# Kernel optimization log

Hardware: AMD Instinct MI355X
Metric: run time of the kernel (lower is better)

Reference implementation:

```python
import jax, jax.numpy as jnp
import numpy as np
import math

D = 256      # d_model
HEADS = 8
PTS = 4      # num_points
L = 6        # num_layers
FF = 1024    # dim_feedforward
B = 8
HS, WS = 100, 100  # feature map -> N = 10000
HD = D // HEADS


def setup_inputs() -> dict:
    key = jax.random.key(0)
    ks = jax.random.split(key, 8)
    w = lambda k, shape, s: jax.random.normal(k, shape, jnp.float32) * s
    z = lambda *shape: jnp.zeros(shape, jnp.float32)
    return {
        "src": jax.random.normal(ks[0], (B, HS * WS, D), jnp.float32),
        "Wv": w(ks[1], (L, D, D), 0.02), "bv": z(L, D),
        "Woff": w(ks[2], (L, D, HEADS * PTS * 2), 0.01), "boff": z(L, HEADS * PTS * 2),
        "Wa": w(ks[3], (L, D, HEADS * PTS), 0.02), "ba": z(L, HEADS * PTS),
        "Wo": w(ks[4], (L, D, D), 0.02), "bo": z(L, D),
        "W1": w(ks[5], (L, D, FF), 0.02), "b1": z(L, FF),
        "W2": w(ks[6], (L, FF, D), 0.02), "b2": z(L, D),
        "g1": jnp.ones((L, D)), "be1": z(L, D),
        "g2": jnp.ones((L, D)), "be2": z(L, D),
        "H": HS, "W": WS,
    }


def pos_encoding_2d(d_model, H, W):
    # standard 2D sine encoding: first half of channels encode y, second half x
    half = d_model // 2
    freqs = jnp.exp(-math.log(10000.0) * jnp.arange(0, half, 2, dtype=jnp.float32) / half)
    ya = jnp.arange(H, dtype=jnp.float32)[:, None] * freqs[None, :]
    xa = jnp.arange(W, dtype=jnp.float32)[:, None] * freqs[None, :]
    pe_y = jnp.stack([jnp.sin(ya), jnp.cos(ya)], -1).reshape(H, half)
    pe_x = jnp.stack([jnp.sin(xa), jnp.cos(xa)], -1).reshape(W, half)
    pe = jnp.concatenate([
        jnp.broadcast_to(pe_y[:, None, :], (H, W, half)),
        jnp.broadcast_to(pe_x[None, :, :], (H, W, half))], -1)
    return pe.reshape(H * W, d_model)


def layer_norm(x, g, b, eps=1e-5):
    m = x.mean(-1, keepdims=True)
    v = ((x - m) ** 2).mean(-1, keepdims=True)
    return (x - m) * jax.lax.rsqrt(v + eps) * g + b


def deform_attn(q, Wv, bv, Woff, boff, Wa, ba, Wo, bo, H, W):
    # single-scale Deformable-DETR attention; q: [B, N, D], N = H*W
    Bq, N, _ = q.shape
    v = (q @ Wv + bv).reshape(Bq, N, HEADS, HD)
    off = (q @ Woff + boff).reshape(Bq, N, HEADS, PTS, 2)          # (dx, dy) in pixels
    attn = jax.nn.softmax((q @ Wa + ba).reshape(Bq, N, HEADS, PTS), axis=-1)
    # reference points: normalized grid cell centers
    ys, xs = jnp.meshgrid(jnp.arange(H, dtype=jnp.float32),
                          jnp.arange(W, dtype=jnp.float32), indexing='ij')
    ref = jnp.stack([(xs.reshape(-1) + 0.5) / W, (ys.reshape(-1) + 0.5) / H], -1)  # [N,2]
    loc = ref[None, :, None, None, :] + off / jnp.array([W, H], jnp.float32)       # [B,N,h,P,2]
    # pixel coords, align_corners=False; border padding via clamping
    px = loc[..., 0] * W - 0.5
    py = loc[..., 1] * H - 0.5
    x0 = jnp.floor(px); y0 = jnp.floor(py)
    wx = px - x0; wy = py - y0
    x0i = jnp.clip(x0.astype(jnp.int32), 0, W - 1); x1i = jnp.clip(x0i + 1, 0, W - 1)
    y0i = jnp.clip(y0.astype(jnp.int32), 0, H - 1); y1i = jnp.clip(y0i + 1, 0, H - 1)
    vbh = v.transpose(0, 2, 1, 3).reshape(Bq * HEADS, N, HD)       # [B*h, N, hd]
    flat = lambda yi, xi: (yi * W + xi).transpose(0, 2, 1, 3).reshape(Bq * HEADS, N * PTS)
    gather = jax.vmap(lambda val, idx: val[idx])                   # [B*h, N*P, hd]
    wxr = wx.transpose(0, 2, 1, 3).reshape(Bq * HEADS, N * PTS, 1)
    wyr = wy.transpose(0, 2, 1, 3).reshape(Bq * HEADS, N * PTS, 1)
    s = (gather(vbh, flat(y0i, x0i)) * (1 - wxr) * (1 - wyr)
         + gather(vbh, flat(y0i, x1i)) * wxr * (1 - wyr)
         + gather(vbh, flat(y1i, x0i)) * (1 - wxr) * wyr
         + gather(vbh, flat(y1i, x1i)) * wxr * wyr)
    s = s.reshape(Bq, HEADS, N, PTS, HD)
    out = jnp.einsum('bhnp,bhnpd->bhnd', attn.transpose(0, 2, 1, 3), s)
    out = out.transpose(0, 2, 1, 3).reshape(Bq, N, D)
    return out @ Wo + bo


def reference(src, Wv, bv, Woff, boff, Wa, ba, Wo, bo, W1, b1, W2, b2,
              g1, be1, g2, be2, H, W):
    x = src + pos_encoding_2d(D, H, W)[None]
    for i in range(L):
        a = deform_attn(x, Wv[i], bv[i], Woff[i], boff[i], Wa[i], ba[i], Wo[i], bo[i], H, W)
        x = layer_norm(x + a, g1[i], be1[i])
        h = jax.nn.gelu(x @ W1[i] + b1[i], approximate=False)
        x = layer_norm(x + (h @ W2[i] + b2[i]), g2[i], be2[i])
    return x
```

## Files before the change

### kernel.cpp

```cpp
#include <hip/hip_runtime.h>
#include <hip/hip_bf16.h>
#include <math.h>

#define Bq   8
#define NPix 10000
#define HH   100
#define WW   100
#define Dm   256
#define NH   8
#define HD   32
#define PTS  4
#define FFd  1024
#define Lnum 6
#define Mrows (Bq * NPix)

typedef short bf16x8 __attribute__((ext_vector_type(8)));
typedef float f32x4 __attribute__((ext_vector_type(4)));
typedef unsigned int uint2v __attribute__((ext_vector_type(2)));

__device__ __forceinline__ float bf2f(unsigned short u) {
    return __uint_as_float(((unsigned)u) << 16);
}
__device__ __forceinline__ unsigned short f2bf(float f) {
    unsigned x = __float_as_uint(f);
    return (unsigned short)((x + 0x7fffu + ((x >> 16) & 1u)) >> 16);
}
__device__ __forceinline__ float gelu_t(float v) {
    float z = 1.5957691216f * (v + 0.044715f * v * v * v);
    float e = __expf(z);
    float th = 1.0f - 2.0f / (e + 1.0f);
    return 0.5f * v * (1.0f + th);
}

__global__ __launch_bounds__(256) void pos_add_kernel(
    const float* __restrict__ src, float* __restrict__ x, short* __restrict__ xb)
{
    int idx = blockIdx.x * 256 + threadIdx.x;
    int c = idx & (Dm - 1);
    int n = (idx >> 8) % NPix;
    int cc = c;
    float coord;
    if (c < 128) { coord = (float)(n / WW); }
    else         { coord = (float)(n % WW); cc = c - 128; }
    int j = cc >> 1;
    float f = __expf(-logf(10000.0f) * (2.0f * (float)j) / 128.0f);
    float arg = coord * f;
    float pe = (cc & 1) ? cosf(arg) : sinf(arg);
    float val = src[idx] + pe;
    x[idx] = val;
    xb[idx] = (short)f2bf(val);
}

__global__ __launch_bounds__(256) void repack_kernel(
    const float* __restrict__ W, short* __restrict__ Wt,
    int K, int N, int outLstride, int nOff)
{
    __shared__ float t[64][65];
    int l  = blockIdx.z;
    int k0 = blockIdx.y * 64, n0 = blockIdx.x * 64;
    const float* Wl = W + (size_t)l * K * N;
    for (int i = threadIdx.x; i < 64 * 64; i += 256) {
        int kk = i >> 6, nn = i & 63;
        float val = 0.0f;
        if (k0 + kk < K && n0 + nn < N) val = Wl[(size_t)(k0 + kk) * N + (n0 + nn)];
        t[kk][nn] = val;
    }
    __syncthreads();
    for (int i = threadIdx.x; i < 64 * 64; i += 256) {
        int nn = i >> 6, kk = i & 63;
        if (n0 + nn < N && k0 + kk < K)
            Wt[(size_t)l * outLstride + (size_t)(nOff + n0 + nn) * K + (k0 + kk)]
                = (short)f2bf(t[kk][nn]);
    }
}

__global__ void bcat_kernel(const float* __restrict__ bv,
                            const float* __restrict__ boff,
                            const float* __restrict__ ba,
                            float* __restrict__ bcat)
{
    int l = blockIdx.x, c = threadIdx.x;
    float v;
    if (c < 256)      v = bv[l * 256 + c];
    else if (c < 320) v = boff[l * 64 + (c - 256)];
    else              v = ba[l * 32 + (c - 320)];
    bcat[l * 352 + c] = v;
}

template<int KI, int MODE>
__global__ __launch_bounds__(256) void gemm_mfma_kernel(
    const short* __restrict__ A, const short* __restrict__ Bt,
    const float* __restrict__ bias, short* __restrict__ Cv,
    float* __restrict__ C2,
    int M, int Nc, int ldc)
{
    constexpr int K = KI * 64;
    __shared__ short As[128 * 64];
    __shared__ short Bs[128 * 64];
    const int tid = threadIdx.x;

    int nwg  = gridDim.x * gridDim.y;
    int orig = blockIdx.y * gridDim.x + blockIdx.x;
    int xcd  = orig & 7, pos = orig >> 3;
    int q = nwg >> 3, r = nwg & 7;
    int flat = (xcd < r ? xcd * (q + 1) : r * (q + 1) + (xcd - r) * q) + pos;
    const int bm = (flat / gridDim.x) * 128;
    const int bn = (flat % gridDim.x) * 128;

    const int w = tid >> 6, l = tid & 63;
    const int wr = (w >> 1) * 64, wc = (w & 1) * 64;
    const int rl = tid >> 3;
    const int cl = tid & 7;
    const int lr = l & 15, lq = l >> 4;

    const short* pA[4]; const short* pB[4];
    #pragma unroll
    for (int p = 0; p < 4; ++p) {
        int row = p * 32 + rl;
        int sc  = cl ^ (row & 7);
        int ga  = bm + row; if (ga > M - 1) ga = M - 1;
        pA[p] = A + (size_t)ga * K + sc * 8;
        int gb  = bn + row; if (gb > Nc - 1) gb = Nc - 1;
        pB[p] = Bt + (size_t)gb * K + sc * 8;
    }

    int xoff[2][4], woff[2][4];
    #pragma unroll
    for (int ks = 0; ks < 2; ++ks)
        #pragma unroll
        for (int m = 0; m < 4; ++m) {
            int ra = wr + m * 16 + lr;
            xoff[ks][m] = ra * 64 + (((ks * 4 + lq) ^ (ra & 7))) * 8;
            int rb = wc + m * 16 + lr;
            woff[ks][m] = rb * 64 + (((ks * 4 + lq) ^ (rb & 7))) * 8;
        }

    f32x4 acc[4][4];
    #pragma unroll
    for (int m = 0; m < 4; ++m)
        #pragma unroll
        for (int n = 0; n < 4; ++n)
            #pragma unroll
            for (int j = 0; j < 4; ++j) acc[m][n][j] = 0.0f;

    #pragma unroll
    for (int kc = 0; kc < KI; ++kc) {
        #pragma unroll
        for (int p = 0; p < 4; ++p) {
            __builtin_amdgcn_global_load_lds((const void*)pA[p],
                (void*)&As[(p * 32 + w * 8) * 64], 16, 0, 0);
            pA[p] += 64;
            __builtin_amdgcn_global_load_lds((const void*)pB[p],
                (void*)&Bs[(p * 32 + w * 8) * 64], 16, 0, 0);
            pB[p] += 64;
        }
        __syncthreads();

        #pragma unroll
        for (int ks = 0; ks < 2; ++ks) {
            bf16x8 wf[4], xf[4];
            #pragma unroll
            for (int m = 0; m < 4; ++m) wf[m] = *(const bf16x8*)&Bs[woff[ks][m]];
            #pragma unroll
            for (int n = 0; n < 4; ++n) xf[n] = *(const bf16x8*)&As[xoff[ks][n]];
            #pragma unroll
            for (int m = 0; m < 4; ++m)
                #pragma unroll
                for (int n = 0; n < 4; ++n)
                    acc[m][n] = __builtin_amdgcn_mfma_f32_16x16x32_bf16(
                        wf[m], xf[n], acc[m][n], 0, 0, 0);
        }
        __syncthreads();
    }

    float4 bi[4];
    #pragma unroll
    for (int m = 0; m < 4; ++m) {
        int colBase = bn + wc + m * 16 + lq * 4;
        bi[m] = (MODE == 2 && colBase >= Nc) ? float4{0,0,0,0}
                                             : *(const float4*)&bias[colBase];
    }

    #pragma unroll
    for (int n = 0; n < 4; ++n) {
        int rr = bm + wr + n * 16 + lr;
        if (rr >= M) continue;
        #pragma unroll
        for (int m = 0; m < 4; ++m) {
            int colBase = bn + wc + m * 16 + lq * 4;
            if (MODE == 2 && colBase >= Nc) continue;
            float o0 = acc[m][n][0] + bi[m].x;
            float o1 = acc[m][n][1] + bi[m].y;
            float o2 = acc[m][n][2] + bi[m].z;
            float o3 = acc[m][n][3] + bi[m].w;
            if (MODE == 0) {
                o0 = gelu_t(o0); o1 = gelu_t(o1); o2 = gelu_t(o2); o3 = gelu_t(o3);
                uint2v pk;
                pk.x = (unsigned)f2bf(o0) | ((unsigned)f2bf(o1) << 16);
                pk.y = (unsigned)f2bf(o2) | ((unsigned)f2bf(o3) << 16);
                *(uint2v*)&Cv[(size_t)rr * ldc + colBase] = pk;
            } else {
                if (colBase < 256) {
                    uint2v pk;
                    pk.x = (unsigned)f2bf(o0) | ((unsigned)f2bf(o1) << 16);
                    pk.y = (unsigned)f2bf(o2) | ((unsigned)f2bf(o3) << 16);
                    *(uint2v*)&Cv[(size_t)rr * 256 + colBase] = pk;
                } else {
                    float4 pk; pk.x = o0; pk.y = o1; pk.z = o2; pk.w = o3;
                    *(float4*)&C2[(size_t)rr * 96 + (colBase - 256)] = pk;
                }
            }
        }
    }
}

template<int KI>
__global__ __launch_bounds__(512) void gemm_ln_kernel(
    const short* __restrict__ A, const short* __restrict__ Bt,
    const float* __restrict__ bias,
    const float* __restrict__ gw, const float* __restrict__ bw,
    float* __restrict__ x, short* __restrict__ xb,
    int M)
{
    constexpr int K = KI * 64;
    __shared__ short As[128 * 64];
    __shared__ short Bs[256 * 64];
    const int tid = threadIdx.x;
    const int bm = blockIdx.x * 128;
    const int w = tid >> 6, l = tid & 63;
    const int lr = l & 15, lq = l >> 4;

    const short* pA[2]; const short* pB[4];
    #pragma unroll
    for (int p = 0; p < 2; ++p) {
        int s = p * 512 + tid;
        int row = s >> 3, cs = s & 7;
        int sc  = cs ^ (row & 7);
        int ga  = bm + row; if (ga > M - 1) ga = M - 1;
        pA[p] = A + (size_t)ga * K + sc * 8;
    }
    #pragma unroll
    for (int p = 0; p < 4; ++p) {
        int s = p * 512 + tid;
        int row = s >> 3, cs = s & 7;
        int sc  = cs ^ (row & 7);
        pB[p] = Bt + (size_t)row * K + sc * 8;
    }

    const int arow = w * 16 + lr;
    int aoff[2];
    #pragma unroll
    for (int ks = 0; ks < 2; ++ks)
        aoff[ks] = arow * 64 + (((ks * 4 + lq) ^ (arow & 7))) * 8;
    int boff[2][16];
    #pragma unroll
    for (int ks = 0; ks < 2; ++ks)
        #pragma unroll
        for (int i = 0; i < 16; ++i) {
            int brow = i * 16 + lr;
            boff[ks][i] = brow * 64 + (((ks * 4 + lq) ^ (brow & 7))) * 8;
        }

    f32x4 acc[16];
    #pragma unroll
    for (int n = 0; n < 16; ++n)
        #pragma unroll
        for (int j = 0; j < 4; ++j) acc[n][j] = 0.0f;

    #pragma unroll
    for (int kc = 0; kc < KI; ++kc) {
        #pragma unroll
        for (int p = 0; p < 2; ++p) {
            __builtin_amdgcn_global_load_lds((const void*)pA[p],
                (void*)&As[(p * 512 + w * 64) * 8], 16, 0, 0);
            pA[p] += 64;
        }
        #pragma unroll
        for (int p = 0; p < 4; ++p) {
            __builtin_amdgcn_global_load_lds((const void*)pB[p],
                (void*)&Bs[(p * 512 + w * 64) * 8], 16, 0, 0);
            pB[p] += 64;
        }
        __syncthreads();

        #pragma unroll
        for (int ks = 0; ks < 2; ++ks) {
            bf16x8 af = *(const bf16x8*)&As[aoff[ks]];
            #pragma unroll
            for (int hb = 0; hb < 2; ++hb) {
                bf16x8 bfr[8];
                #pragma unroll
                for (int i = 0; i < 8; ++i)
                    bfr[i] = *(const bf16x8*)&Bs[boff[ks][hb * 8 + i]];
                #pragma unroll
                for (int i = 0; i < 8; ++i)
                    acc[hb * 8 + i] = __builtin_amdgcn_mfma_f32_16x16x32_bf16(
                        af, bfr[i], acc[hb * 8 + i], 0, 0, 0);
            }
        }
        __syncthreads();
    }

    float bi[16];
    #pragma unroll
    for (int n = 0; n < 16; ++n) bi[n] = bias[n * 16 + lr];

    #pragma unroll
    for (int j = 0; j < 4; ++j) {
        int rr = bm + w * 16 + lq * 4 + j;
        if (rr < M) {
            float tmp[16];
            float sum = 0.0f;
            #pragma unroll
            for (int n = 0; n < 16; ++n) {
                int c = n * 16 + lr;
                float val = acc[n][j] + bi[n] + x[(size_t)rr * 256 + c];
                tmp[n] = val;
                sum += val;
            }
            #pragma unroll
            for (int o = 8; o >= 1; o >>= 1) sum += __shfl_xor(sum, o);
            float mean = sum * (1.0f / 256.0f);
            float vs = 0.0f;
            #pragma unroll
            for (int n = 0; n < 16; ++n) {
                float d = tmp[n] - mean;
                vs += d * d;
            }
            #pragma unroll
            for (int o = 8; o >= 1; o >>= 1) vs += __shfl_xor(vs, o);
            float rstd = rsqrtf(vs * (1.0f / 256.0f) + 1e-5f);
            #pragma unroll
            for (int n = 0; n < 16; ++n) {
                int c = n * 16 + lr;
                float ov = (tmp[n] - mean) * rstd * gw[c] + bw[c];
                x[(size_t)rr * 256 + c] = ov;
                xb[(size_t)rr * 256 + c] = (short)f2bf(ov);
            }
        }
    }
}

__global__ __launch_bounds__(256) void deform_attn_kernel(
    const short* __restrict__ v, const float* __restrict__ comb,
    short* __restrict__ outs)
{
    int g  = blockIdx.x * 16 + (threadIdx.x >> 4);
    int d2 = threadIdx.x & 15;
    int bn = g >> 3, h = g & 7;
    int n  = bn % NPix;
    int row = n / WW, col = n % WW;
    int base_v = (bn / NPix) * NPix;

    const float* cb = comb + (size_t)bn * 96;
    float l0 = cb[64 + h * 4 + 0], l1 = cb[64 + h * 4 + 1];
    float l2 = cb[64 + h * 4 + 2], l3 = cb[64 + h * 4 + 3];
    float mx = fmaxf(fmaxf(l0, l1), fmaxf(l2, l3));
    float e0 = __expf(l0 - mx), e1 = __expf(l1 - mx);
    float e2 = __expf(l2 - mx), e3 = __expf(l3 - mx);
    float inv = 1.0f / (e0 + e1 + e2 + e3);
    float aw[4] = {e0 * inv, e1 * inv, e2 * inv, e3 * inv};

    float acc0 = 0.0f, acc1 = 0.0f;
    size_t chb = (size_t)h * HD + d2 * 2;
    #pragma unroll
    for (int p = 0; p < 4; ++p) {
        float dx = cb[h * 8 + p * 2 + 0];
        float dy = cb[h * 8 + p * 2 + 1];
        float px = (float)col + dx;
        float py = (float)row + dy;
        float x0f = floorf(px), y0f = floorf(py);
        float wx = px - x0f, wy = py - y0f;
        int x0i = min(max((int)x0f, 0), WW - 1);
        int y0i = min(max((int)y0f, 0), HH - 1);
        int x1i = min(x0i + 1, WW - 1);
        int y1i = min(y0i + 1, HH - 1);
        unsigned u00 = *(const unsigned*)&v[(size_t)(base_v + y0i * WW + x0i) * Dm + chb];
        unsigned u01 = *(const unsigned*)&v[(size_t)(base_v + y0i * WW + x1i) * Dm + chb];
        unsigned u10 = *(const unsigned*)&v[(size_t)(base_v + y1i * WW + x0i) * Dm + chb];
        unsigned u11 = *(const unsigned*)&v[(size_t)(base_v + y1i * WW + x1i) * Dm + chb];
        float w00 = (1.0f - wx) * (1.0f - wy), w01 = wx * (1.0f - wy);
        float w10 = (1.0f - wx) * wy,          w11 = wx * wy;
        float s0 = bf2f((unsigned short)u00) * w00 + bf2f((unsigned short)u01) * w01
                 + bf2f((unsigned short)u10) * w10 + bf2f((unsigned short)u11) * w11;
        float s1 = bf2f((unsigned short)(u00 >> 16)) * w00 + bf2f((unsigned short)(u01 >> 16)) * w01
                 + bf2f((unsigned short)(u10 >> 16)) * w10 + bf2f((unsigned short)(u11 >> 16)) * w11;
        acc0 = fmaf(aw[p], s0, acc0);
        acc1 = fmaf(aw[p], s1, acc1);
    }
    unsigned outw = (unsigned)f2bf(acc0) | ((unsigned)f2bf(acc1) << 16);
    *(unsigned*)&outs[(size_t)bn * Dm + chb] = outw;
}

extern "C" void kernel_launch(void* const* d_in, const int* in_sizes, int n_in,
                              void* d_out, int out_size, void* d_ws, size_t ws_size,
                              hipStream_t stream)
{
    const float* src  = (const float*)d_in[0];
    const float* Wv   = (const float*)d_in[1];
    const float* bv   = (const float*)d_in[2];
    const float* Woff = (const float*)d_in[3];
    const float* boff = (const float*)d_in[4];
    const float* Wa   = (const float*)d_in[5];
    const float* ba   = (const float*)d_in[6];
    const float* Wo   = (const float*)d_in[7];
    const float* bo   = (const float*)d_in[8];
    const float* W1   = (const float*)d_in[9];
    const float* b1   = (const float*)d_in[10];
    const float* W2   = (const float*)d_in[11];
    const float* b2   = (const float*)d_in[12];
    const float* g1   = (const float*)d_in[13];
    const float* be1  = (const float*)d_in[14];
    const float* g2   = (const float*)d_in[15];
    const float* be2  = (const float*)d_in[16];

    float* x = (float*)d_out;

    char* cur = (char*)d_ws;
    auto take = [&](size_t bytes) { char* p = cur; cur += (bytes + 255) & ~(size_t)255; return p; };
    short* WcatT = (short*)take((size_t)Lnum * 352 * Dm * 2);
    short* WoT   = (short*)take((size_t)Lnum * Dm * Dm * 2);
    short* W1T   = (short*)take((size_t)Lnum * Dm * FFd * 2);
    short* W2T   = (short*)take((size_t)Lnum * FFd * Dm * 2);
    float* bcat  = (float*)take((size_t)Lnum * 352 * 4);
    short* xb    = (short*)take((size_t)Mrows * Dm * 2);
    size_t fixedB = (size_t)(cur - (char*)d_ws);

    const size_t perRowB = 512 + 512 + 384 + 2048;
    int k = 8;
    while (k > 1 && fixedB + (size_t)k * NPix * perRowB > ws_size) k >>= 1;
    if (fixedB + (size_t)k * NPix * perRowB > ws_size) return;
    const int CM = k * NPix;
    const int nChunks = Bq / k;

    short* v    = (short*)take((size_t)CM * Dm * 2);
    short* sbuf = (short*)take((size_t)CM * Dm * 2);
    float* comb = (float*)take((size_t)CM * 96 * 4);
    short* h    = (short*)take((size_t)CM * FFd * 2);

    repack_kernel<<<dim3(4, 4, Lnum),  256, 0, stream>>>(Wv,   WcatT, Dm,  Dm,  352 * Dm,   0);
    repack_kernel<<<dim3(1, 4, Lnum),  256, 0, stream>>>(Woff, WcatT, Dm,  64,  352 * Dm, 256);
    repack_kernel<<<dim3(1, 4, Lnum),  256, 0, stream>>>(Wa,   WcatT, Dm,  32,  352 * Dm, 320);
    repack_kernel<<<dim3(4, 4, Lnum),  256, 0, stream>>>(Wo,   WoT,   Dm,  Dm,  Dm * Dm,    0);
    repack_kernel<<<dim3(16, 4, Lnum), 256, 0, stream>>>(W1,   W1T,   Dm,  FFd, Dm * FFd,   0);
    repack_kernel<<<dim3(4, 16, Lnum), 256, 0, stream>>>(W2,   W2T,   FFd, Dm,  FFd * Dm,   0);
    bcat_kernel<<<Lnum, 352, 0, stream>>>(bv, boff, ba, bcat);

    pos_add_kernel<<<Mrows, 256, 0, stream>>>(src, x, xb);

    const int gy128 = (CM + 127) / 128;
    const int gLN   = (CM + 127) / 128;

    for (int l = 0; l < Lnum; ++l) {
        const short* WcatT_l = WcatT + (size_t)l * 352 * Dm;
        const short* WoT_l   = WoT   + (size_t)l * Dm * Dm;
        const short* W1T_l   = W1T   + (size_t)l * Dm * FFd;
        const short* W2T_l   = W2T   + (size_t)l * FFd * Dm;

        for (int c = 0; c < nChunks; ++c) {
            size_t rowOff = (size_t)c * CM;
            float* xc  = x  + rowOff * Dm;
            short* xbc = xb + rowOff * Dm;

            gemm_mfma_kernel<4, 2><<<dim3(3, gy128), 256, 0, stream>>>(
                xbc, WcatT_l, bcat + l * 352, v, comb, CM, 352, 0);
            deform_attn_kernel<<<CM / 2, 256, 0, stream>>>(v, comb, sbuf);
            gemm_ln_kernel<4><<<gLN, 512, 0, stream>>>(
                sbuf, WoT_l, bo + l * Dm, g1 + l * Dm, be1 + l * Dm, xc, xbc, CM);
            gemm_mfma_kernel<4, 0><<<dim3(8, gy128), 256, 0, stream>>>(
                xbc, W1T_l, b1 + l * FFd, h, nullptr, CM, FFd, FFd);
            gemm_ln_kernel<16><<<gLN, 512, 0, stream>>>(
                h, W2T_l, b2 + l * Dm, g2 + l * Dm, be2 + l * Dm, xc, xbc, CM);
        }
    }
}
```

Before: 2.193 ms.

## Add dedicated W1 GEMM kernel with 128x256 tiles and XCD-aware block remap

Replaces the generic MFMA GEMM for the FFN up-projection with a specialized 512-thread kernel that computes 128x256 output tiles. It loads A and B through global_load_lds with XOR-swizzled LDS, and fuses bias plus GELU into the bf16 store. It also remaps block IDs so consecutive tiles land on the same XCD, to improve L2 reuse of A rows. The larger tile raises reuse per load but increases register and LDS pressure, which may lower occupancy.

After: 2.312 ms. +5.4%, slower.

```diff
diff --git a/kernel.cpp b/kernel.cpp
--- a/kernel.cpp
+++ b/kernel.cpp
@@ -215,6 +215,123 @@
 }
 
 template<int KI>
+__global__ __launch_bounds__(512) void gemm_w1_kernel(
+    const short* __restrict__ A, const short* __restrict__ Bt,
+    const float* __restrict__ bias, short* __restrict__ Cv,
+    int M, int Nc)
+{
+    constexpr int K = KI * 64;
+    __shared__ short As[128 * 64];
+    __shared__ short Bs[256 * 64];
+    const int tid = threadIdx.x;
+
+    int nwg  = gridDim.x * gridDim.y;
+    int orig = blockIdx.y * gridDim.x + blockIdx.x;
+    int xcd  = orig & 7, pos = orig >> 3;
+    int q = nwg >> 3, r = nwg & 7;
+    int flat = (xcd < r ? xcd * (q + 1) : r * (q + 1) + (xcd - r) * q) + pos;
+    const int bm = (flat / gridDim.x) * 128;
+    const int bn = (flat % gridDim.x) * 256;
+
+    const int w = tid >> 6, l = tid & 63;
+    const int wr = (w >> 2) * 64;
+    const int wc = (w & 3) * 64;
+    const int lr = l & 15, lq = l >> 4;
+
+    const short* pA[2]; const short* pB[4];
+    #pragma unroll
+    for (int p = 0; p < 2; ++p) {
+        int s = p * 512 + tid;
+        int row = s >> 3, cs = s & 7;
+        int sc  = cs ^ (row & 7);
+        int ga  = bm + row; if (ga > M - 1) ga = M - 1;
+        pA[p] = A + (size_t)ga * K + sc * 8;
+    }
+    #pragma unroll
+    for (int p = 0; p < 4; ++p) {
+        int s = p * 512 + tid;
+        int row = s >> 3, cs = s & 7;
+        int sc  = cs ^ (row & 7);
+        pB[p] = Bt + (size_t)(bn + row) * K + sc * 8;
+    }
+
+    int xoff[2][4], woff[2][4];
+    #pragma unroll
+    for (int ks = 0; ks < 2; ++ks)
+        #pragma unroll
+        for (int m = 0; m < 4; ++m) {
+            int ra = wr + m * 16 + lr;
+            xoff[ks][m] = ra * 64 + (((ks * 4 + lq) ^ (ra & 7))) * 8;
+            int rb = wc + m * 16 + lr;
+            woff[ks][m] = rb * 64 + (((ks * 4 + lq) ^ (rb & 7))) * 8;
+        }
+
+    f32x4 acc[4][4];
+    #pragma unroll
+    for (int m = 0; m < 4; ++m)
+        #pragma unroll
+        for (int n = 0; n < 4; ++n)
+            #pragma unroll
+            for (int j = 0; j < 4; ++j) acc[m][n][j] = 0.0f;
+
+    #pragma unroll
+    for (int kc = 0; kc < KI; ++kc) {
+        #pragma unroll
+        for (int p = 0; p < 2; ++p) {
+            __builtin_amdgcn_global_load_lds((const void*)pA[p],
+                (void*)&As[(p * 512 + w * 64) * 8], 16, 0, 0);
+            pA[p] += 64;
+        }
+        #pragma unroll
+        for (int p = 0; p < 4; ++p) {
+            __builtin_amdgcn_global_load_lds((const void*)pB[p],
+                (void*)&Bs[(p * 512 + w * 64) * 8], 16, 0, 0);
+            pB[p] += 64;
+        }
+        __syncthreads();
+
+        #pragma unroll
+        for (int ks = 0; ks < 2; ++ks) {
+            bf16x8 wf[4], xf[4];
+            #pragma unroll
+            for (int m = 0; m < 4; ++m) wf[m] = *(const bf16x8*)&Bs[woff[ks][m]];
+            #pragma unroll
+            for (int n = 0; n < 4; ++n) xf[n] = *(const bf16x8*)&As[xoff[ks][n]];
+            #pragma unroll
+            for (int m = 0; m < 4; ++m)
+                #pragma unroll
+                for (int n = 0; n < 4; ++n)
+                    acc[m][n] = __builtin_amdgcn_mfma_f32_16x16x32_bf16(
+                        wf[m], xf[n], acc[m][n], 0, 0, 0);
+        }
+        __syncthreads();
+    }
+
+    float4 bi[4];
+    #pragma unroll
+    for (int m = 0; m < 4; ++m)
+        bi[m] = *(const float4*)&bias[bn + wc + m * 16 + lq * 4];
+
+    #pragma unroll
+    for (int n = 0; n < 4; ++n) {
+        int rr = bm + wr + n * 16 + lr;
+        if (rr >= M) continue;
+        #pragma unroll
+        for (int m = 0; m < 4; ++m) {
+            int colBase = bn + wc + m * 16 + lq * 4;
+            float o0 = gelu_t(acc[m][n][0] + bi[m].x);
+            float o1 = gelu_t(acc[m][n][1] + bi[m].y);
+            float o2 = gelu_t(acc[m][n][2] + bi[m].z);
+            float o3 = gelu_t(acc[m][n][3] + bi[m].w);
+            uint2v pk;
+            pk.x = (unsigned)f2bf(o0) | ((unsigned)f2bf(o1) << 16);
+            pk.y = (unsigned)f2bf(o2) | ((unsigned)f2bf(o3) << 16);
+            *(uint2v*)&Cv[(size_t)rr * Nc + colBase] = pk;
+        }
+    }
+}
+
+template<int KI>
 __global__ __launch_bounds__(512) void gemm_ln_kernel(
     const short* __restrict__ A, const short* __restrict__ Bt,
     const float* __restrict__ bias,
@@ -467,8 +584,8 @@
             deform_attn_kernel<<<CM / 2, 256, 0, stream>>>(v, comb, sbuf);
             gemm_ln_kernel<4><<<gLN, 512, 0, stream>>>(
                 sbuf, WoT_l, bo + l * Dm, g1 + l * Dm, be1 + l * Dm, xc, xbc, CM);
-            gemm_mfma_kernel<4, 0><<<dim3(8, gy128), 256, 0, stream>>>(
-                xbc, W1T_l, b1 + l * FFd, h, nullptr, CM, FFd, FFd);
+            gemm_w1_kernel<4><<<dim3(4, gy128), 512, 0, stream>>>(
+                xbc, W1T_l, b1 + l * FFd, h, CM, FFd);
             gemm_ln_kernel<16><<<gLN, 512, 0, stream>>>(
                 h, W2T_l, b2 + l * Dm, g2 + l * Dm, be2 + l * Dm, xc, xbc, CM);
         }
```
